# Kernel optimization log

Measured on AMD Instinct MI355X. Metric: run time of the kernel, lower is better.

## Reference

```python
import jax, jax.numpy as jnp
import numpy as np

B, D = 65536, 256      # batch, state dim (= hidden_dims[0])
H1, H2 = 256, 256      # hidden_dims
N_STEPS = 40           # fixed RK4 steps over t in [0, 1]
BN_EPS = 1e-3          # keras BatchNormalization default epsilon


def setup_inputs() -> dict:
    key = jax.random.key(0)
    ks = jax.random.split(key, 8)
    s = 0.05  # small init keeps dynamics smooth/stable
    return {
        "y0": jax.random.normal(ks[0], (B, D), dtype=jnp.float32),
        "W1": jax.random.normal(ks[1], (D, H1), dtype=jnp.float32) * s,
        "b1": jnp.zeros((H1,), jnp.float32),
        "g1": jnp.ones((H1,), jnp.float32),
        "be1": jnp.zeros((H1,), jnp.float32),
        "m1": jnp.zeros((H1,), jnp.float32),
        "v1": jnp.ones((H1,), jnp.float32),
        "W2": jax.random.normal(ks[2], (H1, H2), dtype=jnp.float32) * s,
        "b2": jnp.zeros((H2,), jnp.float32),
        "g2": jnp.ones((H2,), jnp.float32),
        "be2": jnp.zeros((H2,), jnp.float32),
        "m2": jnp.zeros((H2,), jnp.float32),
        "v2": jnp.ones((H2,), jnp.float32),
        "Wo": jax.random.normal(ks[3], (H2, D), dtype=jnp.float32) * s,
        "bo": jnp.zeros((D,), jnp.float32),
    }


def _ode_func(y, W1, b1, g1, be1, m1, v1, W2, b2, g2, be2, m2, v2, Wo, bo):
    # Dense(relu) -> BatchNorm(inference, moving stats) -> Dropout(inactive), x2, then Dense(tanh)
    h = jax.nn.relu(y @ W1 + b1)
    h = g1 * (h - m1) * jax.lax.rsqrt(v1 + BN_EPS) + be1
    h = jax.nn.relu(h @ W2 + b2)
    h = g2 * (h - m2) * jax.lax.rsqrt(v2 + BN_EPS) + be2
    return jnp.tanh(h @ Wo + bo)


def reference(y0, W1, b1, g1, be1, m1, v1, W2, b2, g2, be2, m2, v2, Wo, bo):
    # Integrate dy/dt = f(y) (autonomous) from t=0 to t=1 with fixed-step RK4.
    # (The original uses tfp adaptive BDF; RK4 is the clean deterministic stand-in
    # for the same continuous-time solution.)
    dt = jnp.float32(1.0 / N_STEPS)
    f = lambda y: _ode_func(y, W1, b1, g1, be1, m1, v1, W2, b2, g2, be2, m2, v2, Wo, bo)

    def step(y, _):
        k1 = f(y)
        k2 = f(y + 0.5 * dt * k1)
        k3 = f(y + 0.5 * dt * k2)
        k4 = f(y + dt * k3)
        return y + (dt / 6.0) * (k1 + 2.0 * k2 + 2.0 * k3 + k4), None

    y_final, _ = jax.lax.scan(step, y0, None, length=N_STEPS)
    return y_final
```

## Files before the change

### kernel.cpp

```cpp
#include <hip/hip_runtime.h>


typedef unsigned short u16;
typedef unsigned int   u32;
typedef __attribute__((ext_vector_type(8))) short bf16x8;
typedef __attribute__((ext_vector_type(4))) float f32x4;

#define BN_EPS 1e-3f
#define NROWS  65536
#define BM     128
#define NTHR   512
#define WT_ELEMS 196608

__device__ __forceinline__ u16 f2bf(float f) {
    u32 u = __float_as_uint(f);
    u32 r = u + 0x7FFFu + ((u >> 16) & 1u);
    return (u16)(r >> 16);
}
__device__ __forceinline__ float bf2f(u16 h) {
    return __uint_as_float(((u32)h) << 16);
}
__device__ __forceinline__ float fast_tanh(float x) {
    float e = __expf(2.0f * x);
    return 1.0f - __fdividef(2.0f, e + 1.0f);
}

#define SWZ(row, kb) (((row) << 10) + ((kb) ^ (((row) & 7) << 4)))

__global__ void prep_bias(const float* __restrict__ b2,
                          const float* __restrict__ g1, const float* __restrict__ be1,
                          const float* __restrict__ m1, const float* __restrict__ v1,
                          const float* __restrict__ W2,
                          const float* __restrict__ bo,
                          const float* __restrict__ g2, const float* __restrict__ be2,
                          const float* __restrict__ m2, const float* __restrict__ v2,
                          const float* __restrict__ Wo,
                          float* __restrict__ b2o, float* __restrict__ boo) {
    int t = threadIdx.x;
    if (t < 256) {
        float s = b2[t];
        for (int i = 0; i < 256; ++i) {
            float s1 = g1[i] * rsqrtf(v1[i] + BN_EPS);
            float t1 = be1[i] - s1 * m1[i];
            s += t1 * W2[i * 256 + t];
        }
        b2o[t] = s;
    } else {
        int j = t - 256;
        float s = bo[j];
        for (int i = 0; i < 256; ++i) {
            float s2 = g2[i] * rsqrtf(v2[i] + BN_EPS);
            float t2 = be2[i] - s2 * m2[i];
            s += t2 * Wo[i * 256 + j];
        }
        boo[j] = s;
    }
}

__global__ void prep_weights(const float* __restrict__ W1, const float* __restrict__ W2,
                             const float* __restrict__ Wo,
                             const float* __restrict__ g1, const float* __restrict__ v1,
                             const float* __restrict__ g2, const float* __restrict__ v2,
                             u16* __restrict__ Wt) {
    int tid = blockIdx.x * 256 + threadIdx.x;
    if (tid >= 3 * 768 * 256) return;
    int l   = tid / (768 * 256);
    int r   = tid % (768 * 256);
    int kp  = r >> 8;
    int col = r & 255;
    int ok  = kp & 255;
    float w;
    if (l == 0)      w = W1[ok * 256 + col];
    else if (l == 1) w = W2[ok * 256 + col] * (g1[ok] * rsqrtf(v1[ok] + BN_EPS));
    else             w = Wo[ok * 256 + col] * (g2[ok] * rsqrtf(v2[ok] + BN_EPS));
    u16 hi = f2bf(w);
    u16 out = (kp < 512) ? hi : f2bf(w - bf2f(hi));
    int ks = kp >> 5, gg = (kp >> 3) & 3, j = kp & 7, cb = col >> 4, cc = col & 15;
    Wt[(size_t)l * WT_ELEMS + ks * 8192 + cb * 512 + cc * 32 + gg * 8 + j] = out;
}

template<int MODE>
__global__ __launch_bounds__(NTHR, 2)
void eval_kernel(float* __restrict__ y, float* __restrict__ kbuf, float* __restrict__ acc,
                 const u16* __restrict__ Wt,
                 const float* __restrict__ bias0, const float* __restrict__ bias1,
                 const float* __restrict__ bias2,
                 float c_in, float w_acc) {
    extern __shared__ char smem[];
    const int t = threadIdx.x;
    const size_t rowbase = (size_t)blockIdx.x * BM;

    {
        const int r  = t >> 2;
        const int fc = t & 3;
        const float4* yp = reinterpret_cast<const float4*>(y)    + (rowbase + r) * 64;
        const float4* kp = reinterpret_cast<const float4*>(kbuf) + (rowbase + r) * 64;
#pragma unroll 4
        for (int q = 0; q < 16; ++q) {
            const int fi = fc + (q << 2);
            float4 v = yp[fi];
            if (MODE != 0) {
                const float4 kv = kp[fi];
                v.x = fmaf(c_in, kv.x, v.x);
                v.y = fmaf(c_in, kv.y, v.y);
                v.z = fmaf(c_in, kv.z, v.z);
                v.w = fmaf(c_in, kv.w, v.w);
            }
            ushort4 hi, lo;
            hi.x = f2bf(v.x); lo.x = f2bf(v.x - bf2f(hi.x));
            hi.y = f2bf(v.y); lo.y = f2bf(v.y - bf2f(hi.y));
            hi.z = f2bf(v.z); lo.z = f2bf(v.z - bf2f(hi.z));
            hi.w = f2bf(v.w); lo.w = f2bf(v.w - bf2f(hi.w));
            *reinterpret_cast<ushort4*>(smem + SWZ(r, fi * 8))       = hi;
            *reinterpret_cast<ushort4*>(smem + SWZ(r, 512 + fi * 8)) = lo;
        }
    }
    __syncthreads();

    const int lane = t & 63;
    const int wid  = t >> 6;
    const int wr   = wid >> 2;
    const int wc   = wid & 3;
    const int c16  = lane & 15;
    const int g    = lane >> 4;

    f32x4 accf[4][4];

#pragma unroll
    for (int l = 0; l < 3; ++l) {
        const u16* __restrict__ wt = Wt + (size_t)l * WT_ELEMS;
        const float* bp = (l == 0) ? bias0 : (l == 1) ? bias1 : bias2;

#pragma unroll
        for (int n = 0; n < 4; ++n) {
            const float bv = bp[wc * 64 + n * 16 + c16];
#pragma unroll
            for (int m = 0; m < 4; ++m) accf[m][n] = {bv, bv, bv, bv};
        }

#pragma unroll 2
        for (int ks = 0; ks < 24; ++ks) {
            const int kfull = ks * 32;
            const int kloc  = (kfull >= 512) ? (kfull - 512) : kfull;
            const int kb    = kloc * 2 + g * 16;
            bf16x8 av[4], bv[4];
#pragma unroll
            for (int m = 0; m < 4; ++m) {
                const int row = wr * 64 + m * 16 + c16;
                av[m] = *reinterpret_cast<const bf16x8*>(smem + SWZ(row, kb));
            }
            const u16* wp = wt + (size_t)(ks * 16 + wc * 4) * 512 + c16 * 32 + g * 8;
#pragma unroll
            for (int n = 0; n < 4; ++n)
                bv[n] = *reinterpret_cast<const bf16x8*>(wp + n * 512);
#pragma unroll
            for (int m = 0; m < 4; ++m)
#pragma unroll
                for (int n = 0; n < 4; ++n)
                    accf[m][n] = __builtin_amdgcn_mfma_f32_16x16x32_bf16(
                        av[m], bv[n], accf[m][n], 0, 0, 0);
        }
        __syncthreads();

        if (l < 2) {
#pragma unroll
            for (int m = 0; m < 4; ++m)
#pragma unroll
                for (int n = 0; n < 4; ++n) {
                    const int col = wc * 64 + n * 16 + c16;
#pragma unroll
                    for (int j = 0; j < 4; ++j) {
                        const int row = wr * 64 + m * 16 + g * 4 + j;
                        const float h = fmaxf(accf[m][n][j], 0.0f);
                        const u16 hi = f2bf(h);
                        const u16 lo = f2bf(h - bf2f(hi));
                        *reinterpret_cast<u16*>(smem + SWZ(row, col * 2))       = hi;
                        *reinterpret_cast<u16*>(smem + SWZ(row, 512 + col * 2)) = lo;
                    }
                }
            __syncthreads();
        } else {
#pragma unroll
            for (int m = 0; m < 4; ++m)
#pragma unroll
                for (int n = 0; n < 4; ++n) {
                    const int col = wc * 64 + n * 16 + c16;
#pragma unroll
                    for (int j = 0; j < 4; ++j) {
                        const int row = wr * 64 + m * 16 + g * 4 + j;
                        const size_t gi = (rowbase + row) * 256 + col;
                        const float kv = fast_tanh(accf[m][n][j]);
                        if (MODE == 0)      { kbuf[gi] = kv; acc[gi] = w_acc * kv; }
                        else if (MODE == 1) { kbuf[gi] = kv; acc[gi] += w_acc * kv; }
                        else                { y[gi] = y[gi] + acc[gi] + w_acc * kv; }
                    }
                }
        }
    }
}

extern "C" void kernel_launch(void* const* d_in, const int* in_sizes, int n_in,
                              void* d_out, int out_size, void* d_ws, size_t ws_size,
                              hipStream_t stream) {
    const float* y0  = (const float*)d_in[0];
    const float* W1  = (const float*)d_in[1];
    const float* b1  = (const float*)d_in[2];
    const float* g1  = (const float*)d_in[3];
    const float* be1 = (const float*)d_in[4];
    const float* m1  = (const float*)d_in[5];
    const float* v1  = (const float*)d_in[6];
    const float* W2  = (const float*)d_in[7];
    const float* b2  = (const float*)d_in[8];
    const float* g2  = (const float*)d_in[9];
    const float* be2 = (const float*)d_in[10];
    const float* m2  = (const float*)d_in[11];
    const float* v2  = (const float*)d_in[12];
    const float* Wo  = (const float*)d_in[13];
    const float* bo  = (const float*)d_in[14];

    float* y = (float*)d_out;
    char*  ws = (char*)d_ws;
    const size_t MB = 1024 * 1024;
    float* kbuf = (float*)(ws);
    float* accb = (float*)(ws + 64 * MB);
    u16*   Wt   = (u16*)  (ws + 128 * MB);
    float* b2o  = (float*)(ws + 130 * MB);
    float* boo  = b2o + 256;

    hipFuncSetAttribute(reinterpret_cast<const void*>(&eval_kernel<0>),
                        hipFuncAttributeMaxDynamicSharedMemorySize, 131072);
    hipFuncSetAttribute(reinterpret_cast<const void*>(&eval_kernel<1>),
                        hipFuncAttributeMaxDynamicSharedMemorySize, 131072);
    hipFuncSetAttribute(reinterpret_cast<const void*>(&eval_kernel<2>),
                        hipFuncAttributeMaxDynamicSharedMemorySize, 131072);

    hipMemcpyAsync(y, y0, (size_t)NROWS * 256 * sizeof(float),
                   hipMemcpyDeviceToDevice, stream);
    prep_bias<<<1, 512, 0, stream>>>(b2, g1, be1, m1, v1, W2,
                                     bo, g2, be2, m2, v2, Wo, b2o, boo);
    prep_weights<<<2304, 256, 0, stream>>>(W1, W2, Wo, g1, v1, g2, v2, Wt);

    const float dt = 1.0f / 40.0f;
    const float c2 = 0.5f * dt, c4 = dt;
    const float w16 = dt / 6.0f, w13 = dt / 3.0f;
    const int grid = NROWS / BM;

    for (int s = 0; s < 40; ++s) {
        eval_kernel<0><<<grid, NTHR, 131072, stream>>>(y, kbuf, accb, Wt, b1, b2o, boo, 0.0f, w16);
        eval_kernel<1><<<grid, NTHR, 131072, stream>>>(y, kbuf, accb, Wt, b1, b2o, boo, c2, w13);
        eval_kernel<1><<<grid, NTHR, 131072, stream>>>(y, kbuf, accb, Wt, b1, b2o, boo, c2, w13);
        eval_kernel<2><<<grid, NTHR, 131072, stream>>>(y, kbuf, accb, Wt, b1, b2o, boo, c4, w16);
    }
}
```

Baseline: 19.93 ms.

## Fuse all RK4 steps into one persistent kernel with register-resident state

```diff
diff --git a/kernel.cpp b/kernel.cpp
--- a/kernel.cpp
+++ b/kernel.cpp
@@ -1,4 +1,5 @@
 #include <hip/hip_runtime.h>
+#include <hip/hip_fp16.h>
 
 
 typedef unsigned short u16;
@@ -23,6 +24,14 @@
 __device__ __forceinline__ float fast_tanh(float x) {
     float e = __expf(2.0f * x);
     return 1.0f - __fdividef(2.0f, e + 1.0f);
+}
+__device__ __forceinline__ u32 pack_h2(float a, float b) {
+    __half2 h = __floats2half2_rn(a, b);
+    return *reinterpret_cast<u32*>(&h);
+}
+__device__ __forceinline__ float2 unpack_h2(u32 v) {
+    __half2 h = *reinterpret_cast<__half2*>(&v);
+    return __half22float2(h);
 }
 
 #define SWZ(row, kb) (((row) << 10) + ((kb) ^ (((row) & 7) << 4)))
@@ -79,124 +88,164 @@
     Wt[(size_t)l * WT_ELEMS + ks * 8192 + cb * 512 + cc * 32 + gg * 8 + j] = out;
 }
 
-template<int MODE>
 __global__ __launch_bounds__(NTHR, 2)
-void eval_kernel(float* __restrict__ y, float* __restrict__ kbuf, float* __restrict__ acc,
-                 const u16* __restrict__ Wt,
-                 const float* __restrict__ bias0, const float* __restrict__ bias1,
-                 const float* __restrict__ bias2,
-                 float c_in, float w_acc) {
+void ode_persistent(const float* __restrict__ y0, float* __restrict__ yout,
+                    const u16* __restrict__ Wt,
+                    const float* __restrict__ b1, const float* __restrict__ b2o,
+                    const float* __restrict__ boo) {
     extern __shared__ char smem[];
     const int t = threadIdx.x;
     const size_t rowbase = (size_t)blockIdx.x * BM;
-
-    {
-        const int r  = t >> 2;
-        const int fc = t & 3;
-        const float4* yp = reinterpret_cast<const float4*>(y)    + (rowbase + r) * 64;
-        const float4* kp = reinterpret_cast<const float4*>(kbuf) + (rowbase + r) * 64;
-#pragma unroll 4
-        for (int q = 0; q < 16; ++q) {
-            const int fi = fc + (q << 2);
-            float4 v = yp[fi];
-            if (MODE != 0) {
-                const float4 kv = kp[fi];
-                v.x = fmaf(c_in, kv.x, v.x);
-                v.y = fmaf(c_in, kv.y, v.y);
-                v.z = fmaf(c_in, kv.z, v.z);
-                v.w = fmaf(c_in, kv.w, v.w);
-            }
-            ushort4 hi, lo;
-            hi.x = f2bf(v.x); lo.x = f2bf(v.x - bf2f(hi.x));
-            hi.y = f2bf(v.y); lo.y = f2bf(v.y - bf2f(hi.y));
-            hi.z = f2bf(v.z); lo.z = f2bf(v.z - bf2f(hi.z));
-            hi.w = f2bf(v.w); lo.w = f2bf(v.w - bf2f(hi.w));
-            *reinterpret_cast<ushort4*>(smem + SWZ(r, fi * 8))       = hi;
-            *reinterpret_cast<ushort4*>(smem + SWZ(r, 512 + fi * 8)) = lo;
+    const int lane = t & 63, wid = t >> 6;
+    const int wr = wid >> 2, wc = wid & 3;
+    const int c16 = lane & 15, g = lane >> 4;
+
+    f32x4 Y[4][4];
+    f32x4 K[4][4];
+    u32   A2[4][4][2];
+
+#pragma unroll
+    for (int m = 0; m < 4; ++m)
+#pragma unroll
+        for (int n = 0; n < 4; ++n) {
+            const int col = wc * 64 + n * 16 + c16;
+#pragma unroll
+            for (int j = 0; j < 4; ++j) {
+                const int row = wr * 64 + m * 16 + g * 4 + j;
+                Y[m][n][j] = y0[(rowbase + row) * 256 + col];
+            }
+            K[m][n] = (f32x4){0.f, 0.f, 0.f, 0.f};
+            A2[m][n][0] = 0u; A2[m][n][1] = 0u;
+        }
+
+    const float dt  = 1.0f / 40.0f;
+    const float c2  = 0.5f * dt;
+    const float w16 = dt / 6.0f, w13 = dt / 3.0f;
+
+    for (int it = 0; it < 160; ++it) {
+        const int stage = it & 3;
+        const float c = (stage == 0) ? 0.0f : ((stage == 3) ? dt : c2);
+        const float w = (stage == 1 || stage == 2) ? w13 : w16;
+
+#pragma unroll
+        for (int m = 0; m < 4; ++m)
+#pragma unroll
+            for (int n = 0; n < 4; ++n) {
+                const int col2 = (wc * 64 + n * 16 + c16) * 2;
+#pragma unroll
+                for (int j = 0; j < 4; ++j) {
+                    const int row = wr * 64 + m * 16 + g * 4 + j;
+                    const float x = fmaf(c, K[m][n][j], Y[m][n][j]);
+                    const u32 xb = __float_as_uint(x);
+                    const u16 hi = (u16)(xb >> 16);
+                    const float fl = x - __uint_as_float(xb & 0xFFFF0000u);
+                    *reinterpret_cast<u16*>(smem + SWZ(row, col2))       = hi;
+                    *reinterpret_cast<u16*>(smem + SWZ(row, 512 + col2)) = f2bf(fl);
+                }
+            }
+        __syncthreads();
+
+#pragma unroll 1
+        for (int l = 0; l < 3; ++l) {
+            const u16* __restrict__ wt = Wt + (size_t)l * WT_ELEMS;
+            const float* bp = (l == 0) ? b1 : ((l == 1) ? b2o : boo);
+
+#pragma unroll
+            for (int n = 0; n < 4; ++n) {
+                const float bv = bp[wc * 64 + n * 16 + c16];
+                const f32x4 b4 = {bv, bv, bv, bv};
+#pragma unroll
+                for (int m = 0; m < 4; ++m) K[m][n] = b4;
+            }
+
+#pragma unroll 2
+            for (int ks = 0; ks < 24; ++ks) {
+                const int kfull = ks * 32;
+                const int kloc  = (kfull >= 512) ? (kfull - 512) : kfull;
+                const int kb    = kloc * 2 + g * 16;
+                bf16x8 av[4], bv[4];
+#pragma unroll
+                for (int m = 0; m < 4; ++m) {
+                    const int row = wr * 64 + m * 16 + c16;
+                    av[m] = *reinterpret_cast<const bf16x8*>(smem + SWZ(row, kb));
+                }
+                const u16* wp = wt + (size_t)(ks * 16 + wc * 4) * 512 + c16 * 32 + g * 8;
+#pragma unroll
+                for (int n = 0; n < 4; ++n)
+                    bv[n] = *reinterpret_cast<const bf16x8*>(wp + n * 512);
+#pragma unroll
+                for (int m = 0; m < 4; ++m)
+#pragma unroll
+                    for (int n = 0; n < 4; ++n)
+                        K[m][n] = __builtin_amdgcn_mfma_f32_16x16x32_bf16(
+                            av[m], bv[n], K[m][n], 0, 0, 0);
+            }
+            __syncthreads();
+
+            if (l < 2) {
+#pragma unroll
+                for (int m = 0; m < 4; ++m)
+#pragma unroll
+                    for (int n = 0; n < 4; ++n) {
+                        const int col2 = (wc * 64 + n * 16 + c16) * 2;
+#pragma unroll
+                        for (int j = 0; j < 4; ++j) {
+                            const int row = wr * 64 + m * 16 + g * 4 + j;
+                            const float h = fmaxf(K[m][n][j], 0.0f);
+                            const u32 hb = __float_as_uint(h);
+                            const u16 hi = (u16)(hb >> 16);
+                            const float fl = h - __uint_as_float(hb & 0xFFFF0000u);
+                            *reinterpret_cast<u16*>(smem + SWZ(row, col2))       = hi;
+                            *reinterpret_cast<u16*>(smem + SWZ(row, 512 + col2)) = f2bf(fl);
+                        }
+                    }
+                __syncthreads();
+            }
+        }
+
+        if (stage < 3) {
+#pragma unroll
+            for (int m = 0; m < 4; ++m)
+#pragma unroll
+                for (int n = 0; n < 4; ++n) {
+                    f32x4 kv;
+#pragma unroll
+                    for (int j = 0; j < 4; ++j) kv[j] = fast_tanh(K[m][n][j]);
+                    K[m][n] = kv;
+                    float2 p0 = unpack_h2(A2[m][n][0]);
+                    float2 p1 = unpack_h2(A2[m][n][1]);
+                    A2[m][n][0] = pack_h2(fmaf(w, kv[0], p0.x), fmaf(w, kv[1], p0.y));
+                    A2[m][n][1] = pack_h2(fmaf(w, kv[2], p1.x), fmaf(w, kv[3], p1.y));
+                }
+        } else {
+#pragma unroll
+            for (int m = 0; m < 4; ++m)
+#pragma unroll
+                for (int n = 0; n < 4; ++n) {
+                    float2 p0 = unpack_h2(A2[m][n][0]);
+                    float2 p1 = unpack_h2(A2[m][n][1]);
+                    f32x4 yv = Y[m][n];
+                    yv[0] += p0.x + w * fast_tanh(K[m][n][0]);
+                    yv[1] += p0.y + w * fast_tanh(K[m][n][1]);
+                    yv[2] += p1.x + w * fast_tanh(K[m][n][2]);
+                    yv[3] += p1.y + w * fast_tanh(K[m][n][3]);
+                    Y[m][n] = yv;
+                    A2[m][n][0] = 0u; A2[m][n][1] = 0u;
+                }
         }
     }
-    __syncthreads();
-
-    const int lane = t & 63;
-    const int wid  = t >> 6;
-    const int wr   = wid >> 2;
-    const int wc   = wid & 3;
-    const int c16  = lane & 15;
-    const int g    = lane >> 4;
-
-    f32x4 accf[4][4];
-
-#pragma unroll
-    for (int l = 0; l < 3; ++l) {
-        const u16* __restrict__ wt = Wt + (size_t)l * WT_ELEMS;
-        const float* bp = (l == 0) ? bias0 : (l == 1) ? bias1 : bias2;
-
+
+#pragma unroll
+    for (int m = 0; m < 4; ++m)
 #pragma unroll
         for (int n = 0; n < 4; ++n) {
-            const float bv = bp[wc * 64 + n * 16 + c16];
-#pragma unroll
-            for (int m = 0; m < 4; ++m) accf[m][n] = {bv, bv, bv, bv};
-        }
-
-#pragma unroll 2
-        for (int ks = 0; ks < 24; ++ks) {
-            const int kfull = ks * 32;
-            const int kloc  = (kfull >= 512) ? (kfull - 512) : kfull;
-            const int kb    = kloc * 2 + g * 16;
-            bf16x8 av[4], bv[4];
-#pragma unroll
-            for (int m = 0; m < 4; ++m) {
-                const int row = wr * 64 + m * 16 + c16;
-                av[m] = *reinterpret_cast<const bf16x8*>(smem + SWZ(row, kb));
-            }
-            const u16* wp = wt + (size_t)(ks * 16 + wc * 4) * 512 + c16 * 32 + g * 8;
-#pragma unroll
-            for (int n = 0; n < 4; ++n)
-                bv[n] = *reinterpret_cast<const bf16x8*>(wp + n * 512);
-#pragma unroll
-            for (int m = 0; m < 4; ++m)
-#pragma unroll
-                for (int n = 0; n < 4; ++n)
-                    accf[m][n] = __builtin_amdgcn_mfma_f32_16x16x32_bf16(
-                        av[m], bv[n], accf[m][n], 0, 0, 0);
-        }
-        __syncthreads();
-
-        if (l < 2) {
-#pragma unroll
-            for (int m = 0; m < 4; ++m)
-#pragma unroll
-                for (int n = 0; n < 4; ++n) {
-                    const int col = wc * 64 + n * 16 + c16;
-#pragma unroll
-                    for (int j = 0; j < 4; ++j) {
-                        const int row = wr * 64 + m * 16 + g * 4 + j;
-                        const float h = fmaxf(accf[m][n][j], 0.0f);
-                        const u16 hi = f2bf(h);
-                        const u16 lo = f2bf(h - bf2f(hi));
-                        *reinterpret_cast<u16*>(smem + SWZ(row, col * 2))       = hi;
-                        *reinterpret_cast<u16*>(smem + SWZ(row, 512 + col * 2)) = lo;
-                    }
-                }
-            __syncthreads();
-        } else {
-#pragma unroll
-            for (int m = 0; m < 4; ++m)
-#pragma unroll
-                for (int n = 0; n < 4; ++n) {
-                    const int col = wc * 64 + n * 16 + c16;
-#pragma unroll
-                    for (int j = 0; j < 4; ++j) {
-                        const int row = wr * 64 + m * 16 + g * 4 + j;
-                        const size_t gi = (rowbase + row) * 256 + col;
-                        const float kv = fast_tanh(accf[m][n][j]);
-                        if (MODE == 0)      { kbuf[gi] = kv; acc[gi] = w_acc * kv; }
-                        else if (MODE == 1) { kbuf[gi] = kv; acc[gi] += w_acc * kv; }
-                        else                { y[gi] = y[gi] + acc[gi] + w_acc * kv; }
-                    }
-                }
-        }
-    }
+            const int col = wc * 64 + n * 16 + c16;
+#pragma unroll
+            for (int j = 0; j < 4; ++j) {
+                const int row = wr * 64 + m * 16 + g * 4 + j;
+                yout[(rowbase + row) * 256 + col] = Y[m][n][j];
+            }
+        }
 }
 
 extern "C" void kernel_launch(void* const* d_in, const int* in_sizes, int n_in,
@@ -221,34 +270,16 @@
     float* y = (float*)d_out;
     char*  ws = (char*)d_ws;
     const size_t MB = 1024 * 1024;
-    float* kbuf = (float*)(ws);
-    float* accb = (float*)(ws + 64 * MB);
-    u16*   Wt   = (u16*)  (ws + 128 * MB);
-    float* b2o  = (float*)(ws + 130 * MB);
+    u16*   Wt   = (u16*)(ws);
+    float* b2o  = (float*)(ws + 2 * MB);
     float* boo  = b2o + 256;
 
-    hipFuncSetAttribute(reinterpret_cast<const void*>(&eval_kernel<0>),
+    hipFuncSetAttribute(reinterpret_cast<const void*>(&ode_persistent),
                         hipFuncAttributeMaxDynamicSharedMemorySize, 131072);
-    hipFuncSetAttribute(reinterpret_cast<const void*>(&eval_kernel<1>),
-                        hipFuncAttributeMaxDynamicSharedMemorySize, 131072);
-    hipFuncSetAttribute(reinterpret_cast<const void*>(&eval_kernel<2>),
-                        hipFuncAttributeMaxDynamicSharedMemorySize, 131072);
-
-    hipMemcpyAsync(y, y0, (size_t)NROWS * 256 * sizeof(float),
-                   hipMemcpyDeviceToDevice, stream);
+
     prep_bias<<<1, 512, 0, stream>>>(b2, g1, be1, m1, v1, W2,
                                      bo, g2, be2, m2, v2, Wo, b2o, boo);
     prep_weights<<<2304, 256, 0, stream>>>(W1, W2, Wo, g1, v1, g2, v2, Wt);
 
-    const float dt = 1.0f / 40.0f;
-    const float c2 = 0.5f * dt, c4 = dt;
-    const float w16 = dt / 6.0f, w13 = dt / 3.0f;
-    const int grid = NROWS / BM;
-
-    for (int s = 0; s < 40; ++s) {
-        eval_kernel<0><<<grid, NTHR, 131072, stream>>>(y, kbuf, accb, Wt, b1, b2o, boo, 0.0f, w16);
-        eval_kernel<1><<<grid, NTHR, 131072, stream>>>(y, kbuf, accb, Wt, b1, b2o, boo, c2, w13);
-        eval_kernel<1><<<grid, NTHR, 131072, stream>>>(y, kbuf, accb, Wt, b1, b2o, boo, c2, w13);
-        eval_kernel<2><<<grid, NTHR, 131072, stream>>>(y, kbuf, accb, Wt, b1, b2o, boo, c4, w16);
-    }
-}
+    ode_persistent<<<NROWS / BM, NTHR, 131072, stream>>>(y0, y, Wt, b1, b2o, boo);
+}
```

Measured after the change: 20.08 ms. No clear change (+0.8%).
